# Kernel tuning notes

Measured on AMD Instinct MI355X. Metric: run time of the kernel, lower is better.

Reference implementation:

```python
import jax, jax.numpy as jnp
import numpy as np

N = 50000
E = 800000
FEAT = 128
COND = 64
HID = 128
LAT = 64


def setup_inputs() -> dict:
    key = jax.random.key(0)
    ks = jax.random.split(key, 16)
    inp = {
        "feature": jax.random.normal(ks[0], (N, FEAT), jnp.float32),
        "condition": jax.random.normal(ks[1], (N, COND), jnp.float32),
        "edge_index": jax.random.randint(ks[2], (2, E), 0, N, jnp.int64 if jax.config.jax_enable_x64 else jnp.int32),
        "noise": jax.random.normal(ks[3], (N, LAT), jnp.float32),
        # GCNConv params (glorot-style scale)
        "W_f2h": jax.random.normal(ks[4], (FEAT, HID), jnp.float32) * (1.0 / np.sqrt(FEAT)),
        "b_f2h": jnp.zeros((HID,), jnp.float32),
        "W_c2h": jax.random.normal(ks[5], (COND, HID), jnp.float32) * (1.0 / np.sqrt(COND)),
        "b_c2h": jnp.zeros((HID,), jnp.float32),
        "W_h2h": jax.random.normal(ks[6], (2 * HID, HID), jnp.float32) * (1.0 / np.sqrt(2 * HID)),
        "b_h2h": jnp.zeros((HID,), jnp.float32),
        "W_mean": jax.random.normal(ks[7], (HID, LAT), jnp.float32) * (1.0 / np.sqrt(HID)),
        "b_mean": jnp.zeros((LAT,), jnp.float32),
        "W_logvar": jax.random.normal(ks[8], (HID, LAT), jnp.float32) * (1.0 / np.sqrt(HID)),
        "b_logvar": jnp.zeros((LAT,), jnp.float32),
    }
    return inp


def _gcn_norm(edge_index, n):
    # add self-loops, compute symmetric normalization deg^-1/2 * deg^-1/2
    loop = jnp.arange(n, dtype=edge_index.dtype)
    src = jnp.concatenate([edge_index[0], loop])
    dst = jnp.concatenate([edge_index[1], loop])
    deg = jax.ops.segment_sum(jnp.ones_like(src, jnp.float32), dst, num_segments=n)
    dinv = jnp.where(deg > 0, jax.lax.rsqrt(deg), 0.0)
    norm = dinv[src] * dinv[dst]  # [E+N]
    return src, dst, norm


def _gcn_conv(x, W, b, src, dst, norm, n):
    h = x @ W                                  # [N, out]
    msg = h[src] * norm[:, None]               # gather + scale, [E+N, out]
    out = jax.ops.segment_sum(msg, dst, num_segments=n)
    return out + b


def reference(feature, condition, edge_index, noise,
              W_f2h, b_f2h, W_c2h, b_c2h, W_h2h, b_h2h,
              W_mean, b_mean, W_logvar, b_logvar):
    n = feature.shape[0]
    src, dst, norm = _gcn_norm(edge_index, n)
    f2h = jnp.tanh(_gcn_conv(feature, W_f2h, b_f2h, src, dst, norm, n))
    c2h = jnp.tanh(_gcn_conv(condition, W_c2h, b_c2h, src, dst, norm, n))
    h = jnp.concatenate([f2h, c2h], axis=1)
    h = jnp.tanh(_gcn_conv(h, W_h2h, b_h2h, src, dst, norm, n))
    mean = _gcn_conv(h, W_mean, b_mean, src, dst, norm, n)
    logvar = _gcn_conv(h, W_logvar, b_logvar, src, dst, norm, n)
    z = noise * jnp.exp(0.5 * logvar) + mean
    return (z, mean, logvar)
```

## Files before the change

### kernel.cpp

```cpp
#include <hip/hip_runtime.h>
#include <math.h>

namespace {

constexpr int N = 50000;
constexpr int E = 800000;

typedef __attribute__((ext_vector_type(8))) short short8;
typedef __attribute__((ext_vector_type(4))) float f32x4;
typedef __attribute__((ext_vector_type(2))) float f32x2;


__device__ inline unsigned short f2bf(float f) {
  unsigned int b = __float_as_uint(f);
  unsigned int r = (b + 0x7fffu + ((b >> 16) & 1u)) >> 16;
  return (unsigned short)r;
}
__device__ inline float bf_lo(unsigned int u) { return __uint_as_float(u << 16); }
__device__ inline float bf_hi(unsigned int u) { return __uint_as_float(u & 0xffff0000u); }
__device__ inline unsigned int pack2(float a, float b) {
  return (unsigned int)f2bf(a) | ((unsigned int)f2bf(b) << 16);
}


__device__ inline unsigned int pack4_fp8(float a, float b, float c, float d) {
  int w = 0;
  w = __builtin_amdgcn_cvt_pk_fp8_f32(a, b, w, false);
  w = __builtin_amdgcn_cvt_pk_fp8_f32(c, d, w, true);
  return (unsigned int)w;
}
__device__ inline unsigned char f2fp8(float v) {
  return (unsigned char)(__builtin_amdgcn_cvt_pk_fp8_f32(v, v, 0, false) & 0xff);
}


__global__ void zero_int(int* p, int n) {
  int i = blockIdx.x * blockDim.x + threadIdx.x;
  if (i < n) p[i] = 0;
}

__global__ void count_deg_rank(const int* __restrict__ dst, int* __restrict__ cnt,
                               int* __restrict__ rank, int e) {
  int i = blockIdx.x * blockDim.x + threadIdx.x;
  if (i < e) rank[i] = atomicAdd(&cnt[dst[i]], 1);
}

__global__ void block_sums(const int* __restrict__ cnt, int* __restrict__ bsum, int n) {
  int tid = threadIdx.x;
  int i = blockIdx.x * 256 + tid;
  int v = (i < n) ? cnt[i] : 0;
  for (int off = 32; off > 0; off >>= 1) v += __shfl_down(v, off, 64);
  __shared__ int sred[4];
  if ((tid & 63) == 0) sred[tid >> 6] = v;
  __syncthreads();
  if (tid == 0) bsum[blockIdx.x] = sred[0] + sred[1] + sred[2] + sred[3];
}

__global__ void scan_bsums(int* bsum, int nb) {
  if (threadIdx.x == 0 && blockIdx.x == 0) {
    int run = 0;
    for (int b = 0; b < nb; ++b) { int t = bsum[b]; bsum[b] = run; run += t; }
  }
}

__global__ void scan_chunks(const int* __restrict__ cnt, const int* __restrict__ bsum,
                            int* __restrict__ row_ptr, int n) {
  __shared__ int s[256];
  int tid = threadIdx.x;
  int i = blockIdx.x * 256 + tid;
  int v = (i < n) ? cnt[i] : 0;
  s[tid] = v;
  __syncthreads();
  for (int d = 1; d < 256; d <<= 1) {
    int t = (tid >= d) ? s[tid - d] : 0;
    __syncthreads();
    s[tid] += t;
    __syncthreads();
  }
  if (i < n) {
    int excl = bsum[blockIdx.x] + s[tid] - v;
    row_ptr[i] = excl;
    if (i == n - 1) row_ptr[n] = excl + v;
  }
}

__global__ void compute_dinv(const int* __restrict__ cnt, float* __restrict__ dinv, int n) {
  int i = blockIdx.x * blockDim.x + threadIdx.x;
  if (i < n) dinv[i] = rsqrtf((float)(cnt[i] + 1));
}

__global__ __launch_bounds__(256) void scatter_xcd(const int* __restrict__ src,
                                                   const int* __restrict__ dst,
                                                   const int* __restrict__ rank,
                                                   const int* __restrict__ row_ptr,
                                                   int* __restrict__ csr_src) {
  constexpr int RANGE = (N + 7) / 8;
  int r = blockIdx.x & 7;
  int lo = r * RANGE;
  int hi = lo + RANGE;
  int nb = gridDim.x >> 3;
  int bi = blockIdx.x >> 3;
  for (int e = bi * 256 + threadIdx.x; e < E; e += nb * 256) {
    int d = dst[e];
    if (d >= lo && d < hi) {
      csr_src[row_ptr[d] + rank[e]] = src[e];
    }
  }
}


__global__ void cvt_cond(const float* __restrict__ in, const float* __restrict__ dinv,
                         unsigned char* __restrict__ out, int n) {
  int t = blockIdx.x * blockDim.x + threadIdx.x;
  if (t >= n * 8) return;
  int i = t >> 3, j = t & 7;
  float di = dinv[i];
  const float* s = in + (size_t)i * 64 + j * 8;
  float4 a = *(const float4*)s;
  float4 b = *(const float4*)(s + 4);
  uint2 o;
  o.x = pack4_fp8(di * a.x, di * a.y, di * a.z, di * a.w);
  o.y = pack4_fp8(di * b.x, di * b.y, di * b.z, di * b.w);
  *(uint2*)(out + (size_t)i * 192 + 128 + j * 8) = o;
}

__global__ void pack_w(const float* __restrict__ W1, int s1,
                       const float* __restrict__ W2, int s2, int split,
                       int ksteps, unsigned short* __restrict__ out) {
  int t = blockIdx.x * blockDim.x + threadIdx.x;
  int total = ksteps * 8 * 64;
  if (t >= total) return;
  int ks = t >> 9;
  int ct = (t >> 6) & 7;
  int l = t & 63;
  int k0 = ks * 32 + ((l >> 4) << 3);
  int col = ct * 16 + (l & 15);
  const float* src;
  int c;
  if (col < split) { src = W1 + col; c = s1; }
  else { src = W2 + (col - split); c = s2; }
  unsigned short* o = out + (size_t)t * 8;
#pragma unroll
  for (int i = 0; i < 8; ++i) o[i] = f2bf(src[(size_t)(k0 + i) * c]);
}

__global__ void make_bcat(const float* __restrict__ bm, const float* __restrict__ bl,
                          float* __restrict__ bcat) {
  int j = threadIdx.x;
  if (j < 64) bcat[j] = bm[j];
  else if (j < 128) bcat[j] = bl[j - 64];
}


template <int K, int EPI, bool F32A, int OUT>
__global__ __launch_bounds__(256) void gemm_mfma(const void* __restrict__ Av, int lda,
                                                 const unsigned short* __restrict__ Wp,
                                                 const float* __restrict__ bias_or_scale,
                                                 void* __restrict__ Cv, int ldc, int n) {
  constexpr int KSTEPS = K / 32;
  int tid = threadIdx.x;
  int w = tid >> 6;
  int l = tid & 63;
  int r0 = blockIdx.x * 128 + w * 32;
  int arow = l & 15;
  int kgrp = l >> 4;

  f32x4 acc[2][8];
#pragma unroll
  for (int m = 0; m < 2; ++m)
#pragma unroll
    for (int ct = 0; ct < 8; ++ct) acc[m][ct] = (f32x4)(0.f);

  int ra0 = min(r0 + arow, n - 1);
  int ra1 = min(r0 + 16 + arow, n - 1);

#pragma unroll 1
  for (int ks = 0; ks < KSTEPS; ++ks) {
    short8 a0, a1;
    if (F32A) {
      const float* p0 = (const float*)Av + (size_t)ra0 * lda + kgrp * 8 + ks * 32;
      const float* p1 = (const float*)Av + (size_t)ra1 * lda + kgrp * 8 + ks * 32;
      float4 x0 = *(const float4*)p0, y0 = *(const float4*)(p0 + 4);
      float4 x1 = *(const float4*)p1, y1 = *(const float4*)(p1 + 4);
      unsigned int u[4];
      u[0] = pack2(x0.x, x0.y); u[1] = pack2(x0.z, x0.w);
      u[2] = pack2(y0.x, y0.y); u[3] = pack2(y0.z, y0.w);
      a0 = *(const short8*)u;
      u[0] = pack2(x1.x, x1.y); u[1] = pack2(x1.z, x1.w);
      u[2] = pack2(y1.x, y1.y); u[3] = pack2(y1.z, y1.w);
      a1 = *(const short8*)u;
    } else {
      a0 = *(const short8*)((const unsigned short*)Av + (size_t)ra0 * lda + kgrp * 8 + ks * 32);
      a1 = *(const short8*)((const unsigned short*)Av + (size_t)ra1 * lda + kgrp * 8 + ks * 32);
    }
    const short8* pb = (const short8*)Wp + (size_t)(ks * 8) * 64 + l;
#pragma unroll
    for (int ct = 0; ct < 8; ++ct) {
      short8 b = pb[ct * 64];
      acc[0][ct] = __builtin_amdgcn_mfma_f32_16x16x32_bf16(a0, b, acc[0][ct], 0, 0, 0);
      acc[1][ct] = __builtin_amdgcn_mfma_f32_16x16x32_bf16(a1, b, acc[1][ct], 0, 0, 0);
    }
  }

  int ccol = l & 15;
  int crow = (l >> 4) * 4;
#pragma unroll
  for (int ct = 0; ct < 8; ++ct) {
    int col = ct * 16 + ccol;
    float bv = (EPI == 1) ? bias_or_scale[col] : 0.f;
#pragma unroll
    for (int m = 0; m < 2; ++m) {
#pragma unroll
      for (int r = 0; r < 4; ++r) {
        int row = r0 + m * 16 + crow + r;
        if (row < n) {
          float v = acc[m][ct][r];
          if (EPI == 1) v = tanhf(v + bv);
          if (EPI == 2) v = v * bias_or_scale[row];
          if (OUT == 0)
            ((unsigned short*)Cv)[(size_t)row * ldc + col] = f2bf(v);
          else
            ((unsigned char*)Cv)[(size_t)row * ldc + col] = f2fp8(v);
        }
      }
    }
  }
}


#define ACC8_ADD_FP8(ACC, U)                                            \
  {                                                                     \
    f32x2 t0 = __builtin_amdgcn_cvt_pk_f32_fp8((int)U.x, false);        \
    f32x2 t1 = __builtin_amdgcn_cvt_pk_f32_fp8((int)U.x, true);         \
    f32x2 t2 = __builtin_amdgcn_cvt_pk_f32_fp8((int)U.y, false);        \
    f32x2 t3 = __builtin_amdgcn_cvt_pk_f32_fp8((int)U.y, true);         \
    ACC[0] += t0[0]; ACC[1] += t0[1]; ACC[2] += t1[0]; ACC[3] += t1[1]; \
    ACC[4] += t2[0]; ACC[5] += t2[1]; ACC[6] += t3[0]; ACC[7] += t3[1]; \
  }

#define EDGE_WALK_FP8(LANES)                                            \
  float acc2[8];                                                        \
  _Pragma("unroll")                                                     \
  for (int j = 0; j < 8; ++j) acc2[j] = 0.f;                            \
  int e = e0;                                                           \
  for (; e + 2 <= e1; e += 2) {                                         \
    int s0 = csr_src[e], s1 = csr_src[e + 1];                           \
    uint2 u0 = X8[(size_t)s0 * LANES + lane];                           \
    uint2 u1 = X8[(size_t)s1 * LANES + lane];                           \
    ACC8_ADD_FP8(acc, u0)                                               \
    ACC8_ADD_FP8(acc2, u1)                                              \
  }                                                                     \
  if (e < e1) {                                                         \
    int s0 = csr_src[e];                                                \
    uint2 u0 = X8[(size_t)s0 * LANES + lane];                           \
    ACC8_ADD_FP8(acc, u0)                                               \
  }                                                                     \
  _Pragma("unroll")                                                     \
  for (int j = 0; j < 8; ++j) acc[j] += acc2[j];

#define ACC8_SET_BF(ACC, U)                                \
  ACC[0] = bf_lo(U.x); ACC[1] = bf_hi(U.x);                \
  ACC[2] = bf_lo(U.y); ACC[3] = bf_hi(U.y);                \
  ACC[4] = bf_lo(U.z); ACC[5] = bf_hi(U.z);                \
  ACC[6] = bf_lo(U.w); ACC[7] = bf_hi(U.w);

#define ACC8_ADD_BF(ACC, U)                                \
  ACC[0] += bf_lo(U.x); ACC[1] += bf_hi(U.x);              \
  ACC[2] += bf_lo(U.y); ACC[3] += bf_hi(U.y);              \
  ACC[4] += bf_lo(U.z); ACC[5] += bf_hi(U.z);              \
  ACC[6] += bf_lo(U.w); ACC[7] += bf_hi(U.w);

#define EDGE_WALK_BF(LANES)                                             \
  float acc2[8];                                                        \
  _Pragma("unroll")                                                     \
  for (int j = 0; j < 8; ++j) acc2[j] = 0.f;                            \
  int e = e0;                                                           \
  for (; e + 2 <= e1; e += 2) {                                         \
    int s0 = csr_src[e], s1 = csr_src[e + 1];                           \
    uint4 u0 = X4[(size_t)s0 * LANES + lane];                           \
    uint4 u1 = X4[(size_t)s1 * LANES + lane];                           \
    ACC8_ADD_BF(acc, u0)                                                \
    ACC8_ADD_BF(acc2, u1)                                               \
  }                                                                     \
  if (e < e1) {                                                         \
    int s0 = csr_src[e];                                                \
    uint4 u0 = X4[(size_t)s0 * LANES + lane];                           \
    ACC8_ADD_BF(acc, u0)                                                \
  }                                                                     \
  _Pragma("unroll")                                                     \
  for (int j = 0; j < 8; ++j) acc[j] += acc2[j];


__global__ __launch_bounds__(192) void prop192(const unsigned char* __restrict__ X,
                                               unsigned short* __restrict__ f2h_out,
                                               unsigned short* __restrict__ pc_out,
                                               const int* __restrict__ row_ptr,
                                               const int* __restrict__ csr_src,
                                               const float* __restrict__ dinv,
                                               const float* __restrict__ b_f2h, int n) {
  constexpr int LANES = 24;
  int lane = threadIdx.x % LANES;
  int rloc = threadIdx.x / LANES;
  int i = blockIdx.x * 8 + rloc;
  if (i >= n) return;
  const uint2* X8 = (const uint2*)X;
  float di = dinv[i];
  float acc[8];
#pragma unroll
  for (int j = 0; j < 8; ++j) acc[j] = 0.f;
  {
    uint2 u = X8[(size_t)i * LANES + lane];
    ACC8_ADD_FP8(acc, u)
  }
  int e0 = row_ptr[i], e1 = row_ptr[i + 1];
  EDGE_WALK_FP8(24)
  if (lane < 16) {
    float out[8];
#pragma unroll
    for (int j = 0; j < 8; ++j) out[j] = tanhf(fmaf(di, acc[j], b_f2h[lane * 8 + j]));
    uint4 o;
    o.x = pack2(out[0], out[1]); o.y = pack2(out[2], out[3]);
    o.z = pack2(out[4], out[5]); o.w = pack2(out[6], out[7]);
    *(uint4*)(f2h_out + (size_t)i * 256 + lane * 8) = o;
  } else {
    uint4 o;
    o.x = pack2(di * acc[0], di * acc[1]); o.y = pack2(di * acc[2], di * acc[3]);
    o.z = pack2(di * acc[4], di * acc[5]); o.w = pack2(di * acc[6], di * acc[7]);
    *(uint4*)(pc_out + (size_t)i * 64 + (lane - 16) * 8) = o;
  }
}


__global__ __launch_bounds__(256) void prop128(const unsigned char* __restrict__ X,
                                               unsigned short* __restrict__ Y,
                                               const int* __restrict__ row_ptr,
                                               const int* __restrict__ csr_src,
                                               const float* __restrict__ dinv,
                                               const float* __restrict__ bias, int n) {
  constexpr int LANES = 16;
  int lane = threadIdx.x % LANES;
  int rloc = threadIdx.x / LANES;
  int i = blockIdx.x * 16 + rloc;
  if (i >= n) return;
  const uint2* X8 = (const uint2*)X;
  float di = dinv[i];
  float acc[8];
#pragma unroll
  for (int j = 0; j < 8; ++j) acc[j] = 0.f;
  {
    uint2 u = X8[(size_t)i * LANES + lane];
    ACC8_ADD_FP8(acc, u)
  }
  int e0 = row_ptr[i], e1 = row_ptr[i + 1];
  EDGE_WALK_FP8(16)
  float out[8];
#pragma unroll
  for (int j = 0; j < 8; ++j) out[j] = tanhf(fmaf(di, acc[j], bias[lane * 8 + j]));
  uint4 o;
  o.x = pack2(out[0], out[1]); o.y = pack2(out[2], out[3]);
  o.z = pack2(out[4], out[5]); o.w = pack2(out[6], out[7]);
  *(uint4*)(Y + (size_t)i * 128 + lane * 8) = o;
}


__global__ __launch_bounds__(256) void prop_fin_bf(const unsigned short* __restrict__ X,
                                                   const int* __restrict__ row_ptr,
                                                   const int* __restrict__ csr_src,
                                                   const float* __restrict__ dinv,
                                                   const float* __restrict__ bcat,
                                                   const float* __restrict__ noise,
                                                   float* __restrict__ out, int n) {
  constexpr int LANES = 16;
  int lane = threadIdx.x & 15;
  int rloc = threadIdx.x >> 4;
  int i = blockIdx.x * 16 + rloc;
  if (i >= n) return;
  const uint4* X4 = (const uint4*)X;
  float di = dinv[i];
  float acc[8];
  {
    uint4 u = X4[(size_t)i * LANES + lane];
    ACC8_SET_BF(acc, u)
  }
  int e0 = row_ptr[i], e1 = row_ptr[i + 1];
  EDGE_WALK_BF(16)
  float v[8];
#pragma unroll
  for (int j = 0; j < 8; ++j) v[j] = fmaf(di, acc[j], bcat[lane * 8 + j]);
  float p[8];
#pragma unroll
  for (int j = 0; j < 8; ++j) p[j] = __shfl_xor(v[j], 8);
  size_t n64 = (size_t)n * 64;
  if (lane < 8) {
    const float* nz = noise + (size_t)i * 64 + lane * 8;
    float z[8];
#pragma unroll
    for (int j = 0; j < 8; ++j) z[j] = fmaf(nz[j], expf(0.5f * p[j]), v[j]);
    float* zp = out + (size_t)i * 64 + lane * 8;
    *(float4*)zp = make_float4(z[0], z[1], z[2], z[3]);
    *(float4*)(zp + 4) = make_float4(z[4], z[5], z[6], z[7]);
    float* mp = out + n64 + (size_t)i * 64 + lane * 8;
    *(float4*)mp = make_float4(v[0], v[1], v[2], v[3]);
    *(float4*)(mp + 4) = make_float4(v[4], v[5], v[6], v[7]);
  } else {
    float* lp = out + 2 * n64 + (size_t)i * 64 + (lane - 8) * 8;
    *(float4*)lp = make_float4(v[0], v[1], v[2], v[3]);
    *(float4*)(lp + 4) = make_float4(v[4], v[5], v[6], v[7]);
  }
}

}

extern "C" void kernel_launch(void* const* d_in, const int* in_sizes, int n_in,
                              void* d_out, int out_size, void* d_ws, size_t ws_size,
                              hipStream_t stream) {
  const float* feature   = (const float*)d_in[0];
  const float* condition = (const float*)d_in[1];
  const int*   ei        = (const int*)d_in[2];
  const float* noise     = (const float*)d_in[3];
  const float* W_f2h     = (const float*)d_in[4];
  const float* b_f2h     = (const float*)d_in[5];
  const float* W_c2h     = (const float*)d_in[6];
  const float* b_c2h     = (const float*)d_in[7];
  const float* W_h2h     = (const float*)d_in[8];
  const float* b_h2h     = (const float*)d_in[9];
  const float* W_mean    = (const float*)d_in[10];
  const float* b_mean    = (const float*)d_in[11];
  const float* W_logvar  = (const float*)d_in[12];
  const float* b_logvar  = (const float*)d_in[13];

  const int* src = ei;
  const int* dst = ei + E;

  char* p = (char*)d_ws;
  auto alloc = [&](size_t bytes) {
    char* q = p;
    p += (bytes + 255) & ~(size_t)255;
    return q;
  };
  unsigned char*  buf192 = (unsigned char*)alloc((size_t)N * 192);
  unsigned char*  u2buf  = (unsigned char*)alloc((size_t)N * 128);
  unsigned short* catbuf = (unsigned short*)alloc((size_t)N * 256 * 2);
  unsigned short* Pcbf   = (unsigned short*)alloc((size_t)N * 64 * 2);
  unsigned short* hbuf   = (unsigned short*)alloc((size_t)N * 128 * 2);
  unsigned short* vbuf   = (unsigned short*)alloc((size_t)N * 128 * 2);
  int*   cnt     = (int*)alloc((size_t)N * 4);
  int*   rank    = (int*)alloc((size_t)E * 4);
  int*   row_ptr = (int*)alloc((size_t)(N + 1) * 4);
  int*   csr_src = (int*)alloc((size_t)E * 4);
  int*   bsum    = (int*)alloc(256 * 4);
  float* dinv    = (float*)alloc((size_t)N * 4);
  unsigned short* Wf2h_p = (unsigned short*)alloc(4 * 512 * 8 * 2);
  unsigned short* Wc2h_p = (unsigned short*)alloc(2 * 512 * 8 * 2);
  unsigned short* Wh2h_p = (unsigned short*)alloc(8 * 512 * 8 * 2);
  unsigned short* Wcat_p = (unsigned short*)alloc(4 * 512 * 8 * 2);
  float* bcat    = (float*)alloc(128 * 4);
  (void)ws_size; (void)in_sizes; (void)n_in; (void)out_size;

  int nb = (N + 255) / 256;

  zero_int<<<(N + 255) / 256, 256, 0, stream>>>(cnt, N);
  count_deg_rank<<<(E + 255) / 256, 256, 0, stream>>>(dst, cnt, rank, E);
  block_sums<<<nb, 256, 0, stream>>>(cnt, bsum, N);
  scan_bsums<<<1, 64, 0, stream>>>(bsum, nb);
  scan_chunks<<<nb, 256, 0, stream>>>(cnt, bsum, row_ptr, N);
  compute_dinv<<<(N + 255) / 256, 256, 0, stream>>>(cnt, dinv, N);
  scatter_xcd<<<1024, 256, 0, stream>>>(src, dst, rank, row_ptr, csr_src);

  cvt_cond<<<(N * 8 + 255) / 256, 256, 0, stream>>>(condition, dinv, buf192, N);
  pack_w<<<(4 * 512 + 255) / 256, 256, 0, stream>>>(W_f2h, 128, nullptr, 0, 128, 4, Wf2h_p);
  pack_w<<<(2 * 512 + 255) / 256, 256, 0, stream>>>(W_c2h, 128, nullptr, 0, 128, 2, Wc2h_p);
  pack_w<<<(8 * 512 + 255) / 256, 256, 0, stream>>>(W_h2h, 128, nullptr, 0, 128, 8, Wh2h_p);
  pack_w<<<(4 * 512 + 255) / 256, 256, 0, stream>>>(W_mean, 64, W_logvar, 64, 64, 4, Wcat_p);
  make_bcat<<<1, 128, 0, stream>>>(b_mean, b_logvar, bcat);

  int ggrid = (N + 127) / 128;

  gemm_mfma<128, 2, true, 1><<<ggrid, 256, 0, stream>>>(feature, 128, Wf2h_p, dinv, buf192, 192, N);
  prop192<<<(N + 7) / 8, 192, 0, stream>>>(buf192, catbuf, Pcbf, row_ptr, csr_src, dinv, b_f2h, N);
  gemm_mfma<64, 1, false, 0><<<ggrid, 256, 0, stream>>>(Pcbf, 64, Wc2h_p, b_c2h, catbuf + 128, 256, N);
  gemm_mfma<256, 2, false, 1><<<ggrid, 256, 0, stream>>>(catbuf, 256, Wh2h_p, dinv, u2buf, 128, N);
  prop128<<<(N + 15) / 16, 256, 0, stream>>>(u2buf, hbuf, row_ptr, csr_src, dinv, b_h2h, N);
  gemm_mfma<128, 2, false, 0><<<ggrid, 256, 0, stream>>>(hbuf, 128, Wcat_p, dinv, vbuf, 128, N);
  prop_fin_bf<<<(N + 15) / 16, 256, 0, stream>>>(vbuf, row_ptr, csr_src, dinv, bcat, noise,
                                                 (float*)d_out, N);
}
```

Measured before the change: 292.7 us.

## Widen gather loads to 16 bytes and store mean half in FP8

The propagation kernels now have each lane gather 16 bytes per edge (uint4) and accumulate 16 values, where before it gathered 8 bytes and accumulated 8. Rows are packed so that 5 rows share a 64-lane wave, or 32 rows share a block in prop128. The final GEMM gets a new epilogue mode that writes the mean columns as FP8 and the logvar columns as bf16 in a 192-byte row. The final propagation kernel mixes both formats and uses shuffles to combine exp(logvar) with the mean. This cuts gather bytes and memory transactions per edge, but leaves some lanes idle (4 of 64 per wave), lowers the precision of mean, and raises register pressure.

```diff
diff --git a/kernel.cpp b/kernel.cpp
--- a/kernel.cpp
+++ b/kernel.cpp
@@ -217,10 +217,15 @@
           float v = acc[m][ct][r];
           if (EPI == 1) v = tanhf(v + bv);
           if (EPI == 2) v = v * bias_or_scale[row];
-          if (OUT == 0)
+          if (OUT == 0) {
             ((unsigned short*)Cv)[(size_t)row * ldc + col] = f2bf(v);
-          else
+          } else if (OUT == 1) {
             ((unsigned char*)Cv)[(size_t)row * ldc + col] = f2fp8(v);
+          } else {
+            unsigned char* base = (unsigned char*)Cv + (size_t)row * 192;
+            if (col < 64) base[col] = f2fp8(v);
+            else *(unsigned short*)(base + 64 + (size_t)(col - 64) * 2) = f2bf(v);
+          }
         }
       }
     }
@@ -228,41 +233,21 @@
 }
 
 
-#define ACC8_ADD_FP8(ACC, U)                                            \
+#define ACC16_ADD_FP8(ACC, U)                                           \
   {                                                                     \
     f32x2 t0 = __builtin_amdgcn_cvt_pk_f32_fp8((int)U.x, false);        \
     f32x2 t1 = __builtin_amdgcn_cvt_pk_f32_fp8((int)U.x, true);         \
     f32x2 t2 = __builtin_amdgcn_cvt_pk_f32_fp8((int)U.y, false);        \
     f32x2 t3 = __builtin_amdgcn_cvt_pk_f32_fp8((int)U.y, true);         \
+    f32x2 t4 = __builtin_amdgcn_cvt_pk_f32_fp8((int)U.z, false);        \
+    f32x2 t5 = __builtin_amdgcn_cvt_pk_f32_fp8((int)U.z, true);         \
+    f32x2 t6 = __builtin_amdgcn_cvt_pk_f32_fp8((int)U.w, false);        \
+    f32x2 t7 = __builtin_amdgcn_cvt_pk_f32_fp8((int)U.w, true);         \
     ACC[0] += t0[0]; ACC[1] += t0[1]; ACC[2] += t1[0]; ACC[3] += t1[1]; \
     ACC[4] += t2[0]; ACC[5] += t2[1]; ACC[6] += t3[0]; ACC[7] += t3[1]; \
-  }
-
-#define EDGE_WALK_FP8(LANES)                                            \
-  float acc2[8];                                                        \
-  _Pragma("unroll")                                                     \
-  for (int j = 0; j < 8; ++j) acc2[j] = 0.f;                            \
-  int e = e0;                                                           \
-  for (; e + 2 <= e1; e += 2) {                                         \
-    int s0 = csr_src[e], s1 = csr_src[e + 1];                           \
-    uint2 u0 = X8[(size_t)s0 * LANES + lane];                           \
-    uint2 u1 = X8[(size_t)s1 * LANES + lane];                           \
-    ACC8_ADD_FP8(acc, u0)                                               \
-    ACC8_ADD_FP8(acc2, u1)                                              \
-  }                                                                     \
-  if (e < e1) {                                                         \
-    int s0 = csr_src[e];                                                \
-    uint2 u0 = X8[(size_t)s0 * LANES + lane];                           \
-    ACC8_ADD_FP8(acc, u0)                                               \
-  }                                                                     \
-  _Pragma("unroll")                                                     \
-  for (int j = 0; j < 8; ++j) acc[j] += acc2[j];
-
-#define ACC8_SET_BF(ACC, U)                                \
-  ACC[0] = bf_lo(U.x); ACC[1] = bf_hi(U.x);                \
-  ACC[2] = bf_lo(U.y); ACC[3] = bf_hi(U.y);                \
-  ACC[4] = bf_lo(U.z); ACC[5] = bf_hi(U.z);                \
-  ACC[6] = bf_lo(U.w); ACC[7] = bf_hi(U.w);
+    ACC[8] += t4[0]; ACC[9] += t4[1]; ACC[10] += t5[0]; ACC[11] += t5[1]; \
+    ACC[12] += t6[0]; ACC[13] += t6[1]; ACC[14] += t7[0]; ACC[15] += t7[1]; \
+  }
 
 #define ACC8_ADD_BF(ACC, U)                                \
   ACC[0] += bf_lo(U.x); ACC[1] += bf_hi(U.x);              \
@@ -270,63 +255,68 @@
   ACC[4] += bf_lo(U.z); ACC[5] += bf_hi(U.z);              \
   ACC[6] += bf_lo(U.w); ACC[7] += bf_hi(U.w);
 
-#define EDGE_WALK_BF(LANES)                                             \
-  float acc2[8];                                                        \
-  _Pragma("unroll")                                                     \
-  for (int j = 0; j < 8; ++j) acc2[j] = 0.f;                            \
-  int e = e0;                                                           \
-  for (; e + 2 <= e1; e += 2) {                                         \
-    int s0 = csr_src[e], s1 = csr_src[e + 1];                           \
-    uint4 u0 = X4[(size_t)s0 * LANES + lane];                           \
-    uint4 u1 = X4[(size_t)s1 * LANES + lane];                           \
-    ACC8_ADD_BF(acc, u0)                                                \
-    ACC8_ADD_BF(acc2, u1)                                               \
-  }                                                                     \
-  if (e < e1) {                                                         \
-    int s0 = csr_src[e];                                                \
-    uint4 u0 = X4[(size_t)s0 * LANES + lane];                           \
-    ACC8_ADD_BF(acc, u0)                                                \
-  }                                                                     \
-  _Pragma("unroll")                                                     \
-  for (int j = 0; j < 8; ++j) acc[j] += acc2[j];
-
-
-__global__ __launch_bounds__(192) void prop192(const unsigned char* __restrict__ X,
+
+__global__ __launch_bounds__(256) void prop192(const unsigned char* __restrict__ X,
                                                unsigned short* __restrict__ f2h_out,
                                                unsigned short* __restrict__ pc_out,
                                                const int* __restrict__ row_ptr,
                                                const int* __restrict__ csr_src,
                                                const float* __restrict__ dinv,
                                                const float* __restrict__ b_f2h, int n) {
-  constexpr int LANES = 24;
-  int lane = threadIdx.x % LANES;
-  int rloc = threadIdx.x / LANES;
-  int i = blockIdx.x * 8 + rloc;
+  int wave = threadIdx.x >> 6;
+  int wlane = threadIdx.x & 63;
+  int rrow = wlane / 12;
+  int wl = wlane - rrow * 12;
+  if (rrow >= 5) return;
+  int i = blockIdx.x * 20 + wave * 5 + rrow;
   if (i >= n) return;
-  const uint2* X8 = (const uint2*)X;
+  const uint4* X16 = (const uint4*)X;
   float di = dinv[i];
-  float acc[8];
-#pragma unroll
-  for (int j = 0; j < 8; ++j) acc[j] = 0.f;
+  float acc[16], accB[16];
+#pragma unroll
+  for (int j = 0; j < 16; ++j) { acc[j] = 0.f; accB[j] = 0.f; }
   {
-    uint2 u = X8[(size_t)i * LANES + lane];
-    ACC8_ADD_FP8(acc, u)
+    uint4 u = X16[(size_t)i * 12 + wl];
+    ACC16_ADD_FP8(acc, u)
   }
   int e0 = row_ptr[i], e1 = row_ptr[i + 1];
-  EDGE_WALK_FP8(24)
-  if (lane < 16) {
-    float out[8];
-#pragma unroll
-    for (int j = 0; j < 8; ++j) out[j] = tanhf(fmaf(di, acc[j], b_f2h[lane * 8 + j]));
-    uint4 o;
-    o.x = pack2(out[0], out[1]); o.y = pack2(out[2], out[3]);
-    o.z = pack2(out[4], out[5]); o.w = pack2(out[6], out[7]);
-    *(uint4*)(f2h_out + (size_t)i * 256 + lane * 8) = o;
+  int e = e0;
+  for (; e + 2 <= e1; e += 2) {
+    int s0 = csr_src[e], s1 = csr_src[e + 1];
+    uint4 u0 = X16[(size_t)s0 * 12 + wl];
+    uint4 u1 = X16[(size_t)s1 * 12 + wl];
+    ACC16_ADD_FP8(acc, u0)
+    ACC16_ADD_FP8(accB, u1)
+  }
+  if (e < e1) {
+    int s0 = csr_src[e];
+    uint4 u0 = X16[(size_t)s0 * 12 + wl];
+    ACC16_ADD_FP8(acc, u0)
+  }
+#pragma unroll
+  for (int j = 0; j < 16; ++j) acc[j] += accB[j];
+
+  if (wl < 8) {
+    float out[16];
+#pragma unroll
+    for (int j = 0; j < 16; ++j) out[j] = tanhf(fmaf(di, acc[j], b_f2h[wl * 16 + j]));
+    unsigned short* yp = f2h_out + (size_t)i * 256 + wl * 16;
+    uint4 o0, o1;
+    o0.x = pack2(out[0], out[1]); o0.y = pack2(out[2], out[3]);
+    o0.z = pack2(out[4], out[5]); o0.w = pack2(out[6], out[7]);
+    o1.x = pack2(out[8], out[9]); o1.y = pack2(out[10], out[11]);
+    o1.z = pack2(out[12], out[13]); o1.w = pack2(out[14], out[15]);
+    *(uint4*)yp = o0;
+    *(uint4*)(yp + 8) = o1;
   } else {
-    uint4 o;
-    o.x = pack2(di * acc[0], di * acc[1]); o.y = pack2(di * acc[2], di * acc[3]);
-    o.z = pack2(di * acc[4], di * acc[5]); o.w = pack2(di * acc[6], di * acc[7]);
-    *(uint4*)(pc_out + (size_t)i * 64 + (lane - 16) * 8) = o;
+    unsigned short* yp = pc_out + (size_t)i * 64 + (wl - 8) * 16;
+    uint4 o0, o1;
+    o0.x = pack2(di * acc[0], di * acc[1]); o0.y = pack2(di * acc[2], di * acc[3]);
+    o0.z = pack2(di * acc[4], di * acc[5]); o0.w = pack2(di * acc[6], di * acc[7]);
+    o1.x = pack2(di * acc[8], di * acc[9]); o1.y = pack2(di * acc[10], di * acc[11]);
+    o1.z = pack2(di * acc[12], di * acc[13]); o1.w = pack2(di * acc[14], di * acc[15]);
+    *(uint4*)yp = o0;
+    *(uint4*)(yp + 8) = o1;
   }
 }
 
@@ -337,75 +327,131 @@
                                                const int* __restrict__ csr_src,
                                                const float* __restrict__ dinv,
                                                const float* __restrict__ bias, int n) {
-  constexpr int LANES = 16;
-  int lane = threadIdx.x % LANES;
-  int rloc = threadIdx.x / LANES;
-  int i = blockIdx.x * 16 + rloc;
+  int wl = threadIdx.x & 7;
+  int rloc = threadIdx.x >> 3;
+  int i = blockIdx.x * 32 + rloc;
   if (i >= n) return;
-  const uint2* X8 = (const uint2*)X;
+  const uint4* X16 = (const uint4*)X;
   float di = dinv[i];
-  float acc[8];
-#pragma unroll
-  for (int j = 0; j < 8; ++j) acc[j] = 0.f;
+  float acc[16], accB[16];
+#pragma unroll
+  for (int j = 0; j < 16; ++j) { acc[j] = 0.f; accB[j] = 0.f; }
   {
-    uint2 u = X8[(size_t)i * LANES + lane];
-    ACC8_ADD_FP8(acc, u)
+    uint4 u = X16[(size_t)i * 8 + wl];
+    ACC16_ADD_FP8(acc, u)
   }
   int e0 = row_ptr[i], e1 = row_ptr[i + 1];
-  EDGE_WALK_FP8(16)
-  float out[8];
-#pragma unroll
-  for (int j = 0; j < 8; ++j) out[j] = tanhf(fmaf(di, acc[j], bias[lane * 8 + j]));
-  uint4 o;
-  o.x = pack2(out[0], out[1]); o.y = pack2(out[2], out[3]);
-  o.z = pack2(out[4], out[5]); o.w = pack2(out[6], out[7]);
-  *(uint4*)(Y + (size_t)i * 128 + lane * 8) = o;
-}
-
-
-__global__ __launch_bounds__(256) void prop_fin_bf(const unsigned short* __restrict__ X,
-                                                   const int* __restrict__ row_ptr,
-                                                   const int* __restrict__ csr_src,
-                                                   const float* __restrict__ dinv,
-                                                   const float* __restrict__ bcat,
-                                                   const float* __restrict__ noise,
-                                                   float* __restrict__ out, int n) {
-  constexpr int LANES = 16;
-  int lane = threadIdx.x & 15;
-  int rloc = threadIdx.x >> 4;
-  int i = blockIdx.x * 16 + rloc;
+  int e = e0;
+  for (; e + 2 <= e1; e += 2) {
+    int s0 = csr_src[e], s1 = csr_src[e + 1];
+    uint4 u0 = X16[(size_t)s0 * 8 + wl];
+    uint4 u1 = X16[(size_t)s1 * 8 + wl];
+    ACC16_ADD_FP8(acc, u0)
+    ACC16_ADD_FP8(accB, u1)
+  }
+  if (e < e1) {
+    int s0 = csr_src[e];
+    uint4 u0 = X16[(size_t)s0 * 8 + wl];
+    ACC16_ADD_FP8(acc, u0)
+  }
+#pragma unroll
+  for (int j = 0; j < 16; ++j) acc[j] += accB[j];
+
+  float out[16];
+#pragma unroll
+  for (int j = 0; j < 16; ++j) out[j] = tanhf(fmaf(di, acc[j], bias[wl * 16 + j]));
+  unsigned short* yp = Y + (size_t)i * 128 + wl * 16;
+  uint4 o0, o1;
+  o0.x = pack2(out[0], out[1]); o0.y = pack2(out[2], out[3]);
+  o0.z = pack2(out[4], out[5]); o0.w = pack2(out[6], out[7]);
+  o1.x = pack2(out[8], out[9]); o1.y = pack2(out[10], out[11]);
+  o1.z = pack2(out[12], out[13]); o1.w = pack2(out[14], out[15]);
+  *(uint4*)yp = o0;
+  *(uint4*)(yp + 8) = o1;
+}
+
+
+__global__ __launch_bounds__(256) void prop_fin(const unsigned char* __restrict__ X,
+                                                const int* __restrict__ row_ptr,
+                                                const int* __restrict__ csr_src,
+                                                const float* __restrict__ dinv,
+                                                const float* __restrict__ bcat,
+                                                const float* __restrict__ noise,
+                                                float* __restrict__ out, int n) {
+  int wave = threadIdx.x >> 6;
+  int wlane = threadIdx.x & 63;
+  int rrow = wlane / 12;
+  int wl = wlane - rrow * 12;
+  if (rrow >= 5) return;
+  int i = blockIdx.x * 20 + wave * 5 + rrow;
   if (i >= n) return;
-  const uint4* X4 = (const uint4*)X;
+  int base = rrow * 12;
+  const uint4* X16 = (const uint4*)X;
   float di = dinv[i];
-  float acc[8];
+  bool is_mean = (wl < 4);
+  float acc[16], accB[16];
+#pragma unroll
+  for (int j = 0; j < 16; ++j) { acc[j] = 0.f; accB[j] = 0.f; }
   {
-    uint4 u = X4[(size_t)i * LANES + lane];
-    ACC8_SET_BF(acc, u)
+    uint4 u = X16[(size_t)i * 12 + wl];
+    if (is_mean) { ACC16_ADD_FP8(acc, u) } else { ACC8_ADD_BF(acc, u) }
   }
   int e0 = row_ptr[i], e1 = row_ptr[i + 1];
-  EDGE_WALK_BF(16)
-  float v[8];
-#pragma unroll
-  for (int j = 0; j < 8; ++j) v[j] = fmaf(di, acc[j], bcat[lane * 8 + j]);
-  float p[8];
-#pragma unroll
-  for (int j = 0; j < 8; ++j) p[j] = __shfl_xor(v[j], 8);
+  int e = e0;
+  for (; e + 2 <= e1; e += 2) {
+    int s0 = csr_src[e], s1 = csr_src[e + 1];
+    uint4 u0 = X16[(size_t)s0 * 12 + wl];
+    uint4 u1 = X16[(size_t)s1 * 12 + wl];
+    if (is_mean) {
+      ACC16_ADD_FP8(acc, u0)
+      ACC16_ADD_FP8(accB, u1)
+    } else {
+      ACC8_ADD_BF(acc, u0)
+      ACC8_ADD_BF(accB, u1)
+    }
+  }
+  if (e < e1) {
+    int s0 = csr_src[e];
+    uint4 u0 = X16[(size_t)s0 * 12 + wl];
+    if (is_mean) { ACC16_ADD_FP8(acc, u0) } else { ACC8_ADD_BF(acc, u0) }
+  }
+#pragma unroll
+  for (int j = 0; j < 16; ++j) acc[j] += accB[j];
+
+  int lvo = (wl >= 4) ? (wl - 4) : 0;
+  const float* nz = noise + (size_t)i * 64 + lvo * 8;
+  float lv[8], t[8];
+#pragma unroll
+  for (int j = 0; j < 8; ++j) {
+    lv[j] = fmaf(di, acc[j], bcat[64 + lvo * 8 + j]);
+    t[j] = nz[j] * expf(0.5f * lv[j]);
+  }
+  int mo = is_mean ? wl : 0;
+  float mv[16];
+#pragma unroll
+  for (int j = 0; j < 16; ++j) mv[j] = fmaf(di, acc[j], bcat[mo * 16 + j]);
+  float z[16];
+#pragma unroll
+  for (int j = 0; j < 16; ++j) {
+    float tj = __shfl(t[j & 7], base + 4 + wl * 2 + (j >> 3));
+    z[j] = mv[j] + tj;
+  }
   size_t n64 = (size_t)n * 64;
-  if (lane < 8) {
-    const float* nz = noise + (size_t)i * 64 + lane * 8;
-    float z[8];
-#pragma unroll
-    for (int j = 0; j < 8; ++j) z[j] = fmaf(nz[j], expf(0.5f * p[j]), v[j]);
-    float* zp = out + (size_t)i * 64 + lane * 8;
+  if (is_mean) {
+    float* zp = out + (size_t)i * 64 + wl * 16;
     *(float4*)zp = make_float4(z[0], z[1], z[2], z[3]);
     *(float4*)(zp + 4) = make_float4(z[4], z[5], z[6], z[7]);
-    float* mp = out + n64 + (size_t)i * 64 + lane * 8;
-    *(float4*)mp = make_float4(v[0], v[1], v[2], v[3]);
-    *(float4*)(mp + 4) = make_float4(v[4], v[5], v[6], v[7]);
+    *(float4*)(zp + 8) = make_float4(z[8], z[9], z[10], z[11]);
+    *(float4*)(zp + 12) = make_float4(z[12], z[13], z[14], z[15]);
+    float* mp = out + n64 + (size_t)i * 64 + wl * 16;
+    *(float4*)mp = make_float4(mv[0], mv[1], mv[2], mv[3]);
+    *(float4*)(mp + 4) = make_float4(mv[4], mv[5], mv[6], mv[7]);
+    *(float4*)(mp + 8) = make_float4(mv[8], mv[9], mv[10], mv[11]);
+    *(float4*)(mp + 12) = make_float4(mv[12], mv[13], mv[14], mv[15]);
   } else {
-    float* lp = out + 2 * n64 + (size_t)i * 64 + (lane - 8) * 8;
-    *(float4*)lp = make_float4(v[0], v[1], v[2], v[3]);
-    *(float4*)(lp + 4) = make_float4(v[4], v[5], v[6], v[7]);
+    float* lp = out + 2 * n64 + (size_t)i * 64 + lvo * 8;
+    *(float4*)lp = make_float4(lv[0], lv[1], lv[2], lv[3]);
+    *(float4*)(lp + 4) = make_float4(lv[4], lv[5], lv[6], lv[7]);
   }
 }
 
@@ -440,10 +486,10 @@
   };
   unsigned char*  buf192 = (unsigned char*)alloc((size_t)N * 192);
   unsigned char*  u2buf  = (unsigned char*)alloc((size_t)N * 128);
+  unsigned char*  vbuf   = (unsigned char*)alloc((size_t)N * 192);
   unsigned short* catbuf = (unsigned short*)alloc((size_t)N * 256 * 2);
   unsigned short* Pcbf   = (unsigned short*)alloc((size_t)N * 64 * 2);
   unsigned short* hbuf   = (unsigned short*)alloc((size_t)N * 128 * 2);
-  unsigned short* vbuf   = (unsigned short*)alloc((size_t)N * 128 * 2);
   int*   cnt     = (int*)alloc((size_t)N * 4);
   int*   rank    = (int*)alloc((size_t)E * 4);
   int*   row_ptr = (int*)alloc((size_t)(N + 1) * 4);
@@ -477,11 +523,11 @@
   int ggrid = (N + 127) / 128;
 
   gemm_mfma<128, 2, true, 1><<<ggrid, 256, 0, stream>>>(feature, 128, Wf2h_p, dinv, buf192, 192, N);
-  prop192<<<(N + 7) / 8, 192, 0, stream>>>(buf192, catbuf, Pcbf, row_ptr, csr_src, dinv, b_f2h, N);
+  prop192<<<(N + 19) / 20, 256, 0, stream>>>(buf192, catbuf, Pcbf, row_ptr, csr_src, dinv, b_f2h, N);
   gemm_mfma<64, 1, false, 0><<<ggrid, 256, 0, stream>>>(Pcbf, 64, Wc2h_p, b_c2h, catbuf + 128, 256, N);
   gemm_mfma<256, 2, false, 1><<<ggrid, 256, 0, stream>>>(catbuf, 256, Wh2h_p, dinv, u2buf, 128, N);
-  prop128<<<(N + 15) / 16, 256, 0, stream>>>(u2buf, hbuf, row_ptr, csr_src, dinv, b_h2h, N);
-  gemm_mfma<128, 2, false, 0><<<ggrid, 256, 0, stream>>>(hbuf, 128, Wcat_p, dinv, vbuf, 128, N);
-  prop_fin_bf<<<(N + 15) / 16, 256, 0, stream>>>(vbuf, row_ptr, csr_src, dinv, bcat, noise,
-                                                 (float*)d_out, N);
-}
+  prop128<<<(N + 31) / 32, 256, 0, stream>>>(u2buf, hbuf, row_ptr, csr_src, dinv, b_h2h, N);
+  gemm_mfma<128, 2, false, 2><<<ggrid, 256, 0, stream>>>(hbuf, 128, Wcat_p, dinv, vbuf, 192, N);
+  prop_fin<<<(N + 19) / 20, 256, 0, stream>>>(vbuf, row_ptr, csr_src, dinv, bcat, noise,
+                                              (float*)d_out, N);
+}
```

Measured after the change: 291.6 us. Within noise of the previous version (-0.4%).
